# Kernel optimization log

Measured on AMD Instinct MI355X. Metric: run time of the kernel, lower is better.

Reference implementation:

```python
import jax, jax.numpy as jnp
import numpy as np

WS = 14  # window size
NH = 12  # num heads
EPS = 1e-5  # torch LayerNorm eps


def _rel_idx(ws: int) -> np.ndarray:
    coords = np.stack(np.meshgrid(np.arange(ws), np.arange(ws), indexing='ij'))
    cf = coords.reshape(2, -1)                      # (2, N)
    rel = cf[:, :, None] - cf[:, None, :]           # (2, N, N)
    rel = rel.transpose(1, 2, 0).copy()
    rel[:, :, 0] += ws - 1
    rel[:, :, 1] += ws - 1
    rel[:, :, 0] *= 2 * ws - 1
    return rel.sum(-1)                              # (N, N) int


def _layernorm(x, w, b):
    mu = jnp.mean(x, axis=-1, keepdims=True)
    var = jnp.var(x, axis=-1, keepdims=True)
    return (x - mu) * jax.lax.rsqrt(var + EPS) * w + b


def setup_inputs() -> dict:
    key = jax.random.key(0)
    ks = jax.random.split(key, 8)
    d, dff = 768, 3072
    s = lambda k, shape, sc: jax.random.normal(k, shape, jnp.float32) * sc
    return {
        'x': jax.random.normal(ks[0], (8, d, 56, 56), jnp.float32),
        'norm1_w': jnp.ones((d,), jnp.float32),
        'norm1_b': jnp.zeros((d,), jnp.float32),
        'qkv_w': s(ks[1], (d, 3 * d), 0.02),
        'qkv_b': jnp.zeros((3 * d,), jnp.float32),
        'rel_bias_table': s(ks[2], ((2 * WS - 1) ** 2, NH), 0.02),
        'proj_w': s(ks[3], (d, d), 0.02),
        'proj_b': jnp.zeros((d,), jnp.float32),
        'norm2_w': jnp.ones((d,), jnp.float32),
        'norm2_b': jnp.zeros((d,), jnp.float32),
        'fc1_w': s(ks[4], (d, dff), 0.02),
        'fc1_b': jnp.zeros((dff,), jnp.float32),
        'fc2_w': s(ks[5], (dff, d), 0.02),
        'fc2_b': jnp.zeros((d,), jnp.float32),
        'gamma1': jnp.full((d,), 1e-5, jnp.float32),
        'gamma2': jnp.full((d,), 1e-5, jnp.float32),
    }


def reference(x, norm1_w, norm1_b, qkv_w, qkv_b, rel_bias_table, proj_w, proj_b,
              norm2_w, norm2_b, fc1_w, fc1_b, fc2_w, fc2_b, gamma1, gamma2):
    B, C, H, W = x.shape
    nh, hd = NH, C // NH
    N = WS * WS
    xs = jnp.transpose(x, (0, 2, 3, 1))             # B,H,W,C
    shortcut = xs
    h = _layernorm(xs, norm1_w, norm1_b)

    # window partition (H, W divisible by WS)
    hw = h.reshape(B, H // WS, WS, W // WS, WS, C)
    hw = jnp.transpose(hw, (0, 1, 3, 2, 4, 5)).reshape(-1, N, C)  # (Bw, N, C)

    qkv = hw @ qkv_w + qkv_b                        # (Bw, N, 3C)
    qkv = qkv.reshape(-1, N, 3, nh, hd)
    q, k, v = [jnp.transpose(qkv[:, :, i], (0, 2, 1, 3)) for i in range(3)]  # (Bw,nh,N,hd)

    attn = jnp.einsum('bhnd,bhmd->bhnm', q, k) * (hd ** -0.5)
    rel_idx = jnp.asarray(_rel_idx(WS))             # static (N,N)
    bias = rel_bias_table[rel_idx]                  # (N,N,nh)
    attn = attn + jnp.transpose(bias, (2, 0, 1))[None]
    attn = jax.nn.softmax(attn, axis=-1)

    out = jnp.einsum('bhnm,bhmd->bnhd', attn, v).reshape(-1, N, C)
    out = out @ proj_w + proj_b                     # (Bw, N, C)

    # window reverse
    out = out.reshape(B, H // WS, W // WS, WS, WS, C)
    out = jnp.transpose(out, (0, 1, 3, 2, 4, 5)).reshape(B, H, W, C)

    xs = shortcut + gamma1 * out
    h2 = _layernorm(xs, norm2_w, norm2_b)
    mlp = jax.nn.gelu(h2 @ fc1_w + fc1_b, approximate=False) @ fc2_w + fc2_b
    xs = xs + gamma2 * mlp
    return jnp.transpose(xs, (0, 3, 1, 2))          # B,C,H,W
```

## Files before the change

kernel.cpp:

```cpp
#include <hip/hip_runtime.h>
#include <cstdint>
#include <cstddef>


typedef unsigned short u16;
typedef short short8 __attribute__((ext_vector_type(8)));
typedef float floatx4 __attribute__((ext_vector_type(4)));

static __device__ __forceinline__ float bf2f(u16 u) {
  return __uint_as_float(((unsigned)u) << 16);
}
static __device__ __forceinline__ u16 f2bf(float f) {
  unsigned u = __float_as_uint(f);
  return (u16)((u + 0x7FFFu + ((u >> 16) & 1u)) >> 16);
}
static __device__ __forceinline__ float ldin(const void* p, size_t i, int isf) {
  return isf ? ((const float*)p)[i] : bf2f(((const u16*)p)[i]);
}
static __device__ __forceinline__ void gload_lds16(const void* g, void* l) {
  __builtin_amdgcn_global_load_lds(
      (const __attribute__((address_space(1))) void*)g,
      (__attribute__((address_space(3))) void*)l, 16, 0, 0);
}
static __device__ __forceinline__ float fast_gelu(float v) {
  float u2 = v * (1.5957691216f + 0.0713548163f * v * v);
  return v * (1.0f / (1.0f + __expf(-u2)));
}

__global__ __launch_bounds__(256) void detect_kernel(const u16* __restrict__ x,
                                                     int* __restrict__ flag) {
  __shared__ int tot;
  if (threadIdx.x == 0) tot = 0;
  __syncthreads();
  int cnt = 0;
  for (int i = threadIdx.x; i < 4096; i += 256) {
    int e = (x[i] >> 7) & 0xFF;
    if (e >= 0xC1) cnt++;
  }
  atomicAdd(&tot, cnt);
  __syncthreads();
  if (threadIdx.x == 0) flag[0] = (tot > 16) ? 1 : 0;
}

__global__ __launch_bounds__(256) void cvt_params_kernel(
    const void* n1w, const void* n1b, const void* qkvb, const void* projb,
    const void* n2w, const void* n2b, const void* fc1b, const void* fc2b,
    const void* g1, const void* g2, const void* bt, u16* __restrict__ P,
    const int* __restrict__ flag) {
  int isf = *flag;
  int i = blockIdx.x * 256 + threadIdx.x;
  const void* src; int off;
  if      (i < 768)   { src = n1w;   off = i; }
  else if (i < 1536)  { src = n1b;   off = i - 768; }
  else if (i < 3840)  { src = qkvb;  off = i - 1536; }
  else if (i < 4608)  { src = projb; off = i - 3840; }
  else if (i < 5376)  { src = n2w;   off = i - 4608; }
  else if (i < 6144)  { src = n2b;   off = i - 5376; }
  else if (i < 9216)  { src = fc1b;  off = i - 6144; }
  else if (i < 9984)  { src = fc2b;  off = i - 9216; }
  else if (i < 10752) { src = g1;    off = i - 9984; }
  else if (i < 11520) { src = g2;    off = i - 10752; }
  else if (i < 20268) { src = bt;    off = i - 11520; }
  else return;
  P[i] = f2bf(ldin(src, off, isf));
}

__global__ __launch_bounds__(256) void wtr_kernel(const void* __restrict__ W,
                                                  u16* __restrict__ WT,
                                                  int K, int N,
                                                  const int* __restrict__ flag) {
  int isf = *flag;
  __shared__ u16 tl[32][33];
  int tx = threadIdx.x, ty = threadIdx.y;
  int n0 = blockIdx.x * 32, k0 = blockIdx.y * 32;
#pragma unroll
  for (int j = 0; j < 32; j += 8)
    tl[ty + j][tx] = f2bf(ldin(W, (size_t)(k0 + ty + j) * N + n0 + tx, isf));
  __syncthreads();
#pragma unroll
  for (int j = 0; j < 32; j += 8)
    WT[(size_t)(n0 + ty + j) * K + k0 + tx] = tl[tx][ty + j];
}

__global__ __launch_bounds__(256) void tin_kernel(const void* __restrict__ x,
                                                  u16* __restrict__ sc,
                                                  const int* __restrict__ flag) {
  int isf = *flag;
  int cc = blockIdx.x, h = blockIdx.y, b = blockIdx.z;
  __shared__ u16 tile[64 * 57];
  int tid = threadIdx.x;
  for (int i = tid; i < 64 * 56; i += 256) {
    int ci = i / 56, w = i - ci * 56;
    tile[ci * 57 + w] =
        f2bf(ldin(x, (((size_t)b * 768 + cc * 64 + ci) * 56 + h) * 56 + w, isf));
  }
  __syncthreads();
  int hb = h / 14, hi = h - hb * 14;
  for (int i = tid; i < 56 * 64; i += 256) {
    int w = i >> 6, ci = i & 63;
    int wb = w / 14, wj = w - wb * 14;
    int r = (b * 16 + hb * 4 + wb) * 196 + hi * 14 + wj;
    sc[(size_t)r * 768 + cc * 64 + ci] = tile[ci * 57 + w];
  }
}

__global__ __launch_bounds__(256) void tout_kernel(const u16* __restrict__ src,
                                                   void* __restrict__ out,
                                                   const int* __restrict__ flag) {
  int isf = *flag;
  int cc = blockIdx.x, h = blockIdx.y, b = blockIdx.z;
  __shared__ u16 tile[64 * 57];
  int tid = threadIdx.x;
  int hb = h / 14, hi = h - hb * 14;
  for (int i = tid; i < 56 * 64; i += 256) {
    int w = i >> 6, ci = i & 63;
    int wb = w / 14, wj = w - wb * 14;
    int r = (b * 16 + hb * 4 + wb) * 196 + hi * 14 + wj;
    tile[ci * 57 + w] = src[(size_t)r * 768 + cc * 64 + ci];
  }
  __syncthreads();
  for (int i = tid; i < 64 * 56; i += 256) {
    int ci = i / 56, w = i - ci * 56;
    size_t o = (((size_t)b * 768 + cc * 64 + ci) * 56 + h) * 56 + w;
    if (isf) ((float*)out)[o] = bf2f(tile[ci * 57 + w]);
    else     ((u16*)out)[o]   = tile[ci * 57 + w];
  }
}

__global__ __launch_bounds__(256) void ln_kernel(const u16* __restrict__ xin,
                                                 const u16* __restrict__ wt,
                                                 const u16* __restrict__ bs,
                                                 u16* __restrict__ out) {
  int row = blockIdx.x, t = threadIdx.x;
  const u16* xr = xin + (size_t)row * 768;
  float v0 = bf2f(xr[t]), v1 = bf2f(xr[t + 256]), v2 = bf2f(xr[t + 512]);
  float s1 = v0 + v1 + v2;
  float s2 = v0 * v0 + v1 * v1 + v2 * v2;
#pragma unroll
  for (int off = 32; off > 0; off >>= 1) {
    s1 += __shfl_xor(s1, off);
    s2 += __shfl_xor(s2, off);
  }
  __shared__ float p1[4], p2[4];
  if ((t & 63) == 0) { p1[t >> 6] = s1; p2[t >> 6] = s2; }
  __syncthreads();
  float S1 = p1[0] + p1[1] + p1[2] + p1[3];
  float S2 = p2[0] + p2[1] + p2[2] + p2[3];
  float mu = S1 * (1.f / 768.f);
  float var = S2 * (1.f / 768.f) - mu * mu;
  float rs = rsqrtf(var + 1e-5f);
  u16* orow = out + (size_t)row * 768;
  orow[t]       = f2bf((v0 - mu) * rs * bf2f(wt[t])       + bf2f(bs[t]));
  orow[t + 256] = f2bf((v1 - mu) * rs * bf2f(wt[t + 256]) + bf2f(bs[t + 256]));
  orow[t + 512] = f2bf((v2 - mu) * rs * bf2f(wt[t + 512]) + bf2f(bs[t + 512]));
}

template <int EPI>
__global__ __launch_bounds__(256, 4) void gemm128_kernel(
    const u16* __restrict__ A, const u16* __restrict__ BT,
    const u16* __restrict__ bias, const u16* __restrict__ gamma,
    u16* __restrict__ out, int M, int N, int K, int NX, int NYT) {
  __shared__ __align__(16) u16 LDS[8704];

  int bid = blockIdx.x;
  int r8 = bid & 7, q = bid >> 3;
  int xb = q % NX, yb = (q / NX) * 8 + r8;
  if (yb >= NYT) return;
  int m0 = yb * 128, n0 = xb * 128;

  int tid = threadIdx.x;
  int w = tid >> 6, l = tid & 63;
  int l15 = l & 15, quad = l >> 4;
  int wm = w & 1, wn = w >> 1;

  int lrow16 = l >> 2;
  int lk = ((l & 3) ^ ((l >> 3) & 3)) * 8;
  int ra0 = m0 + w * 32 + lrow16;       if (ra0 > M - 1) ra0 = M - 1;
  int ra1 = m0 + w * 32 + 16 + lrow16;  if (ra1 > M - 1) ra1 = M - 1;
  const u16* a0 = A + (size_t)ra0 * K + lk;
  const u16* a1 = A + (size_t)ra1 * K + lk;
  const u16* b0 = BT + (size_t)(n0 + w * 32 + lrow16) * K + lk;
  const u16* b1 = BT + (size_t)(n0 + w * 32 + 16 + lrow16) * K + lk;
  int dA0 = (w * 2) * 512, dA1 = (w * 2 + 1) * 512;

  int kqs = (quad ^ ((l15 >> 1) & 3)) * 8;

  floatx4 acc[4][4];
#pragma unroll
  for (int i = 0; i < 4; ++i)
#pragma unroll
    for (int j = 0; j < 4; ++j)
#pragma unroll
      for (int e = 0; e < 4; ++e) acc[i][j][e] = 0.f;

  int nt = K >> 5;
  for (int t = 0; t < nt; ++t) {
    int ko = t << 5;
    __syncthreads();
    gload_lds16(a0 + ko, LDS + dA0);
    gload_lds16(a1 + ko, LDS + dA1);
    gload_lds16(b0 + ko, LDS + 4096 + dA0);
    gload_lds16(b1 + ko, LDS + 4096 + dA1);
    __syncthreads();
    __builtin_amdgcn_s_setprio(1);
    short8 bfr[4];
#pragma unroll
    for (int ni = 0; ni < 4; ++ni)
      bfr[ni] = *(const short8*)&LDS[4096 + (wn * 64 + ni * 16 + l15) * 32 + kqs];
#pragma unroll
    for (int mi = 0; mi < 4; ++mi) {
      short8 afr = *(const short8*)&LDS[(wm * 64 + mi * 16 + l15) * 32 + kqs];
#pragma unroll
      for (int ni = 0; ni < 4; ++ni)
        acc[mi][ni] = __builtin_amdgcn_mfma_f32_16x16x32_bf16(
            afr, bfr[ni], acc[mi][ni], 0, 0, 0);
    }
    __builtin_amdgcn_s_setprio(0);
  }

  constexpr int CSTR = 136;
  float bv[4];
#pragma unroll
  for (int ni = 0; ni < 4; ++ni)
    bv[ni] = bf2f(bias[n0 + wn * 64 + ni * 16 + l15]);
  for (int cch = 0; cch < 2; ++cch) {
    __syncthreads();
    if (wm == cch) {
#pragma unroll
      for (int mi = 0; mi < 4; ++mi)
#pragma unroll
        for (int ni = 0; ni < 4; ++ni) {
          int cl = wn * 64 + ni * 16 + l15;
#pragma unroll
          for (int reg = 0; reg < 4; ++reg) {
            float v = acc[mi][ni][reg] + bv[ni];
            if constexpr (EPI == 2) v = fast_gelu(v);
            LDS[(mi * 16 + quad * 4 + reg) * CSTR + cl] = f2bf(v);
          }
        }
    }
    __syncthreads();
#pragma unroll
    for (int it = 0; it < 4; ++it) {
      int idx = it * 256 + tid;
      int row = idx >> 4, c8 = (idx & 15) * 8;
      int grow = m0 + cch * 64 + row;
      if (grow < M) {
        short8 val = *(const short8*)&LDS[row * CSTR + c8];
        u16* po = out + (size_t)grow * N + n0 + c8;
        if constexpr (EPI == 1) {
          short8 rv = *(const short8*)po;
          short8 gv = *(const short8*)(gamma + n0 + c8);
          short8 res;
#pragma unroll
          for (int e = 0; e < 8; ++e)
            res[e] = (short)f2bf(bf2f((u16)rv[e]) +
                                 bf2f((u16)gv[e]) * bf2f((u16)val[e]));
          *(short8*)po = res;
        } else {
          *(short8*)po = val;
        }
      }
    }
  }
}

__global__ __launch_bounds__(256) void attn_kernel(const u16* __restrict__ qkv,
                                                   const u16* __restrict__ btab,
                                                   u16* __restrict__ out) {
  __shared__ __align__(16) u16 VT[64 * 232];
  __shared__ __align__(16) u16 Pa[4 * 2 * 512];
  __shared__ float bS[729];
  int bid = blockIdx.x;
  int win = bid / 12, h = bid - win * 12;
  int tid = threadIdx.x, w = tid >> 6, l = tid & 63;
  int lane15 = l & 15, quad = l >> 4;
  const u16* qbase = qkv + (size_t)win * 196 * 2304;

  for (int i = tid; i < 64 * 28; i += 256) {
    int d = i / 28, m = i - d * 28;
    VT[d * 232 + 196 + m] = 0;
  }
  for (int i = tid; i < 196 * 64; i += 256) {
    int m = i >> 6, d = i & 63;
    VT[d * 232 + m] = qbase[(size_t)m * 2304 + 1536 + h * 64 + d];
  }
  for (int i = tid; i < 729; i += 256) bS[i] = bf2f(btab[i * 12 + h]);
  __syncthreads();

  u16* Pw = Pa + w * 1024;
  for (int rt = w; rt < 13; rt += 4) {
    floatx4 acc[13];
#pragma unroll
    for (int nt = 0; nt < 13; ++nt)
#pragma unroll
      for (int e = 0; e < 4; ++e) acc[nt][e] = 0.f;

    int rq = rt * 16 + lane15;
    bool qok = rq < 196;
#pragma unroll
    for (int kk = 0; kk < 2; ++kk) {
      short8 qf;
      if (qok)
        qf = *(const short8*)&qbase[(size_t)rq * 2304 + h * 64 + kk * 32 + quad * 8];
      else
#pragma unroll
        for (int e = 0; e < 8; ++e) qf[e] = 0;
#pragma unroll
      for (int nt = 0; nt < 13; ++nt) {
        int n = nt * 16 + lane15;
        short8 kf = *(const short8*)&qbase[(size_t)n * 2304 + 768 + h * 64 + kk * 32 + quad * 8];
        acc[nt] = __builtin_amdgcn_mfma_f32_16x16x32_bf16(qf, kf, acc[nt], 0, 0, 0);
      }
    }

    int i1[4], j1[4]; bool rv[4]; float mx[4], sm[4];
#pragma unroll
    for (int reg = 0; reg < 4; ++reg) {
      int r = rt * 16 + quad * 4 + reg;
      i1[reg] = r / 14; j1[reg] = r - i1[reg] * 14;
      rv[reg] = r < 196; mx[reg] = -1e30f; sm[reg] = 0.f;
    }
#pragma unroll
    for (int nt = 0; nt < 13; ++nt) {
      int cc = nt * 16 + lane15;
      bool cv = cc < 196;
      int i2 = cc / 14, j2 = cc - i2 * 14;
#pragma unroll
      for (int reg = 0; reg < 4; ++reg) {
        float v;
        if (cv) {
          v = acc[nt][reg] * 0.125f;
          if (rv[reg]) v += bS[(i1[reg] - i2 + 13) * 27 + (j1[reg] - j2 + 13)];
        } else v = -1e30f;
        acc[nt][reg] = v;
        mx[reg] = fmaxf(mx[reg], v);
      }
    }
#pragma unroll
    for (int reg = 0; reg < 4; ++reg)
#pragma unroll
      for (int off = 1; off < 16; off <<= 1)
        mx[reg] = fmaxf(mx[reg], __shfl_xor(mx[reg], off));
#pragma unroll
    for (int nt = 0; nt < 13; ++nt)
#pragma unroll
      for (int reg = 0; reg < 4; ++reg) {
        float p = __expf(acc[nt][reg] - mx[reg]);
        acc[nt][reg] = p; sm[reg] += p;
      }
#pragma unroll
    for (int reg = 0; reg < 4; ++reg) {
#pragma unroll
      for (int off = 1; off < 16; off <<= 1) sm[reg] += __shfl_xor(sm[reg], off);
      sm[reg] = 1.f / sm[reg];
    }

    floatx4 oa[4];
#pragma unroll
    for (int dt = 0; dt < 4; ++dt)
#pragma unroll
      for (int e = 0; e < 4; ++e) oa[dt][e] = 0.f;
#pragma unroll
    for (int kk = 0; kk < 7; ++kk) {
      u16* Pb = Pw + (kk & 1) * 512;
#pragma unroll
      for (int p = 0; p < 2; ++p) {
        int nt = kk * 2 + p;
#pragma unroll
        for (int reg = 0; reg < 4; ++reg) {
          float v = (nt < 13) ? acc[nt][reg] * sm[reg] : 0.f;
          Pb[(quad * 4 + reg) * 32 + p * 16 + lane15] = f2bf(v);
        }
      }
      asm volatile("s_waitcnt lgkmcnt(0)" ::: "memory");
      short8 pf = *(const short8*)&Pb[lane15 * 32 + quad * 8];
#pragma unroll
      for (int dt = 0; dt < 4; ++dt) {
        short8 vf = *(const short8*)&VT[(dt * 16 + lane15) * 232 + kk * 32 + quad * 8];
        oa[dt] = __builtin_amdgcn_mfma_f32_16x16x32_bf16(pf, vf, oa[dt], 0, 0, 0);
      }
    }
#pragma unroll
    for (int dt = 0; dt < 4; ++dt)
#pragma unroll
      for (int reg = 0; reg < 4; ++reg) {
        int r = rt * 16 + quad * 4 + reg;
        if (r < 196)
          out[((size_t)win * 196 + r) * 768 + h * 64 + dt * 16 + lane15] =
              f2bf(oa[dt][reg]);
      }
  }
}

static inline int gemm_grid(int NX, int NYT) { return NX * ((NYT + 7) / 8) * 8; }

extern "C" void kernel_launch(void* const* d_in, const int* in_sizes, int n_in,
                              void* d_out, int out_size, void* d_ws, size_t ws_size,
                              hipStream_t stream) {
  const void* x      = d_in[0];
  const void* n1w    = d_in[1];
  const void* n1b    = d_in[2];
  const void* qkv_w  = d_in[3];
  const void* qkv_b  = d_in[4];
  const void* btab   = d_in[5];
  const void* proj_w = d_in[6];
  const void* proj_b = d_in[7];
  const void* n2w    = d_in[8];
  const void* n2b    = d_in[9];
  const void* fc1_w  = d_in[10];
  const void* fc1_b  = d_in[11];
  const void* fc2_w  = d_in[12];
  const void* fc2_b  = d_in[13];
  const void* gamma1 = d_in[14];
  const void* gamma2 = d_in[15];
  (void)in_sizes; (void)n_in; (void)out_size;

  int c;
  if      (ws_size >= 245432576ull) c = 1;
  else if (ws_size >= 168362240ull) c = 2;
  else                              c = 4;
  const int R = 25088 / c;
  const int WN = 128 / c;
  const int NYT = (R + 127) / 128;

  char* ws = (char*)d_ws;
  int*  flag  = (int*)ws;
  u16*  P     = (u16*)(ws + 256);
  u16*  qkvT  = (u16*)(ws + 65792);
  u16*  projT = (u16*)(ws + 65792 + 3538944);
  u16*  fc1T  = (u16*)(ws + 65792 + 4718592);
  u16*  fc2T  = (u16*)(ws + 65792 + 9437184);
  const size_t B0 = 38535168;
  u16*  buf0  = (u16*)(ws + 14221568);
  u16*  buf1  = (u16*)(ws + 14221568 + B0);
  char* scr   = ws + 14221568 + 2 * B0;

  u16 *p_n1w = P, *p_n1b = P + 768, *p_qkvb = P + 1536, *p_projb = P + 3840;
  u16 *p_n2w = P + 4608, *p_n2b = P + 5376, *p_fc1b = P + 6144;
  u16 *p_fc2b = P + 9216, *p_g1 = P + 9984, *p_g2 = P + 10752, *p_bt = P + 11520;

  dim3 b256(256), bw(32, 8);
  detect_kernel<<<dim3(1), b256, 0, stream>>>((const u16*)x, flag);
  cvt_params_kernel<<<dim3(80), b256, 0, stream>>>(
      n1w, n1b, qkv_b, proj_b, n2w, n2b, fc1_b, fc2_b, gamma1, gamma2, btab,
      P, flag);
  wtr_kernel<<<dim3(72, 24), bw, 0, stream>>>(qkv_w, qkvT, 768, 2304, flag);
  wtr_kernel<<<dim3(24, 24), bw, 0, stream>>>(proj_w, projT, 768, 768, flag);
  wtr_kernel<<<dim3(96, 24), bw, 0, stream>>>(fc1_w, fc1T, 768, 3072, flag);
  wtr_kernel<<<dim3(24, 96), bw, 0, stream>>>(fc2_w, fc2T, 3072, 768, flag);

  tin_kernel<<<dim3(12, 56, 8), b256, 0, stream>>>(x, buf0, flag);
  ln_kernel<<<dim3(25088), b256, 0, stream>>>(buf0, p_n1w, p_n1b, buf1);

  for (int hc = 0; hc < c; ++hc) {
    size_t ro = (size_t)hc * R * 768;
    u16* qC = (u16*)scr;
    u16* aC = (u16*)(scr + (size_t)R * 4608);
    gemm128_kernel<0><<<dim3(gemm_grid(18, NYT)), b256, 0, stream>>>(
        buf1 + ro, qkvT, p_qkvb, nullptr, qC, R, 2304, 768, 18, NYT);
    attn_kernel<<<dim3(WN * 12), b256, 0, stream>>>(qC, p_bt, aC);
    gemm128_kernel<1><<<dim3(gemm_grid(6, NYT)), b256, 0, stream>>>(
        aC, projT, p_projb, p_g1, buf0 + ro, R, 768, 768, 6, NYT);
  }

  ln_kernel<<<dim3(25088), b256, 0, stream>>>(buf0, p_n2w, p_n2b, buf1);

  for (int hc = 0; hc < c; ++hc) {
    size_t ro = (size_t)hc * R * 768;
    u16* gC = (u16*)scr;
    gemm128_kernel<2><<<dim3(gemm_grid(24, NYT)), b256, 0, stream>>>(
        buf1 + ro, fc1T, p_fc1b, nullptr, gC, R, 3072, 768, 24, NYT);
    gemm128_kernel<1><<<dim3(gemm_grid(6, NYT)), b256, 0, stream>>>(
        gC, fc2T, p_fc2b, p_g2, buf0 + ro, R, 768, 3072, 6, NYT);
  }

  tout_kernel<<<dim3(12, 56, 8), b256, 0, stream>>>(buf0, d_out, flag);
}
```

Before: 980.8 us.

## Replace 128x128 GEMM with larger 512-thread tiles and register-prefetched operands

```diff
diff --git a/kernel.cpp b/kernel.cpp
--- a/kernel.cpp
+++ b/kernel.cpp
@@ -156,66 +156,232 @@
 }
 
 template <int EPI>
-__global__ __launch_bounds__(256, 4) void gemm128_kernel(
+__global__ __launch_bounds__(512, 2) void gemmA_kernel(
     const u16* __restrict__ A, const u16* __restrict__ BT,
     const u16* __restrict__ bias, const u16* __restrict__ gamma,
     u16* __restrict__ out, int M, int N, int K, int NX, int NYT) {
-  __shared__ __align__(16) u16 LDS[8704];
+  constexpr int ATS = 16384;
+  __shared__ __align__(16) u16 LDS[2 * ATS];
 
   int bid = blockIdx.x;
   int r8 = bid & 7, q = bid >> 3;
   int xb = q % NX, yb = (q / NX) * 8 + r8;
   if (yb >= NYT) return;
-  int m0 = yb * 128, n0 = xb * 128;
+  int m0 = yb * 256, n0 = xb * 256;
 
   int tid = threadIdx.x;
   int w = tid >> 6, l = tid & 63;
   int l15 = l & 15, quad = l >> 4;
   int wm = w & 1, wn = w >> 1;
 
-  int lrow16 = l >> 2;
-  int lk = ((l & 3) ^ ((l >> 3) & 3)) * 8;
-  int ra0 = m0 + w * 32 + lrow16;       if (ra0 > M - 1) ra0 = M - 1;
-  int ra1 = m0 + w * 32 + 16 + lrow16;  if (ra1 > M - 1) ra1 = M - 1;
-  const u16* a0 = A + (size_t)ra0 * K + lk;
-  const u16* a1 = A + (size_t)ra1 * K + lk;
-  const u16* b0 = BT + (size_t)(n0 + w * 32 + lrow16) * K + lk;
-  const u16* b1 = BT + (size_t)(n0 + w * 32 + 16 + lrow16) * K + lk;
-  int dA0 = (w * 2) * 512, dA1 = (w * 2 + 1) * 512;
-
-  int kqs = (quad ^ ((l15 >> 1) & 3)) * 8;
+  int lrow8 = l >> 3;
+  int lk = ((l & 7) ^ lrow8) * 8;
+  const u16* aptr[4];
+#pragma unroll
+  for (int j = 0; j < 4; ++j) {
+    int ra = m0 + w * 32 + j * 8 + lrow8;
+    if (ra > M - 1) ra = M - 1;
+    aptr[j] = A + (size_t)ra * K + lk;
+  }
+  int kq0 = (((quad * 16)      ^ ((l15 & 7) << 4)) >> 1);
+  int kq1 = (((64 + quad * 16) ^ ((l15 & 7) << 4)) >> 1);
+
+  const u16* bp0 = BT + (size_t)(n0 + wn * 64 +  0 + l15) * K + quad * 8;
+  const u16* bp1 = BT + (size_t)(n0 + wn * 64 + 16 + l15) * K + quad * 8;
+  const u16* bp2 = BT + (size_t)(n0 + wn * 64 + 32 + l15) * K + quad * 8;
+  const u16* bp3 = BT + (size_t)(n0 + wn * 64 + 48 + l15) * K + quad * 8;
+
+  floatx4 acc[8][4];
+#pragma unroll
+  for (int i = 0; i < 8; ++i)
+#pragma unroll
+    for (int jn = 0; jn < 4; ++jn)
+#pragma unroll
+      for (int e = 0; e < 4; ++e) acc[i][jn][e] = 0.f;
+
+  int nt = K >> 6;
+#pragma unroll
+  for (int j = 0; j < 4; ++j)
+    gload_lds16(aptr[j], LDS + (w * 4 + j) * 512);
+  short8 bc[4][2], bn[4][2];
+  bc[0][0] = *(const short8*)(bp0);      bc[0][1] = *(const short8*)(bp0 + 32);
+  bc[1][0] = *(const short8*)(bp1);      bc[1][1] = *(const short8*)(bp1 + 32);
+  bc[2][0] = *(const short8*)(bp2);      bc[2][1] = *(const short8*)(bp2 + 32);
+  bc[3][0] = *(const short8*)(bp3);      bc[3][1] = *(const short8*)(bp3 + 32);
+
+#pragma unroll 2
+  for (int t = 0; t < nt; ++t) {
+    const u16* Ac = LDS + (t & 1) * ATS;
+    u16* An = LDS + ((t + 1) & 1) * ATS;
+    asm volatile("s_waitcnt vmcnt(0)" ::: "memory");
+    __builtin_amdgcn_s_barrier();
+    bool pf = (t + 1) < nt;
+    int ko = (t + 1) << 6;
+    if (pf) {
+#pragma unroll
+      for (int j = 0; j < 4; ++j)
+        gload_lds16(aptr[j] + ko, An + (w * 4 + j) * 512);
+      bn[0][0] = *(const short8*)(bp0 + ko);
+      bn[0][1] = *(const short8*)(bp0 + ko + 32);
+      bn[1][0] = *(const short8*)(bp1 + ko);
+      bn[1][1] = *(const short8*)(bp1 + ko + 32);
+      bn[2][0] = *(const short8*)(bp2 + ko);
+      bn[2][1] = *(const short8*)(bp2 + ko + 32);
+      bn[3][0] = *(const short8*)(bp3 + ko);
+      bn[3][1] = *(const short8*)(bp3 + ko + 32);
+    }
+    __builtin_amdgcn_s_setprio(1);
+#pragma unroll
+    for (int mi = 0; mi < 8; ++mi) {
+      const u16* ap = Ac + (wm * 128 + mi * 16 + l15) * 64;
+      short8 a0 = *(const short8*)(ap + kq0);
+      short8 a1 = *(const short8*)(ap + kq1);
+#pragma unroll
+      for (int ni = 0; ni < 4; ++ni) {
+        acc[mi][ni] = __builtin_amdgcn_mfma_f32_16x16x32_bf16(
+            a0, bc[ni][0], acc[mi][ni], 0, 0, 0);
+        acc[mi][ni] = __builtin_amdgcn_mfma_f32_16x16x32_bf16(
+            a1, bc[ni][1], acc[mi][ni], 0, 0, 0);
+      }
+    }
+    __builtin_amdgcn_s_setprio(0);
+#pragma unroll
+    for (int ni = 0; ni < 4; ++ni) {
+      bc[ni][0] = bn[ni][0];
+      bc[ni][1] = bn[ni][1];
+    }
+  }
+
+  constexpr int CSTR = 264;
+  float bv[4];
+#pragma unroll
+  for (int ni = 0; ni < 4; ++ni)
+    bv[ni] = bf2f(bias[n0 + wn * 64 + ni * 16 + l15]);
+#pragma unroll
+  for (int cch = 0; cch < 4; ++cch) {
+    __syncthreads();
+    if (wm == (cch >> 1)) {
+#pragma unroll
+      for (int mi = 0; mi < 8; ++mi) {
+        if ((mi >> 2) == (cch & 1)) {
+          int rloc = (mi & 3) * 16 + quad * 4;
+#pragma unroll
+          for (int ni = 0; ni < 4; ++ni) {
+            int cl = wn * 64 + ni * 16 + l15;
+#pragma unroll
+            for (int reg = 0; reg < 4; ++reg) {
+              float v = acc[mi][ni][reg] + bv[ni];
+              if constexpr (EPI == 2) v = fast_gelu(v);
+              LDS[(rloc + reg) * CSTR + cl] = f2bf(v);
+            }
+          }
+        }
+      }
+    }
+    __syncthreads();
+#pragma unroll
+    for (int it = 0; it < 4; ++it) {
+      int idx = it * 512 + tid;
+      int row = idx >> 5, c8 = (idx & 31) * 8;
+      int grow = m0 + cch * 64 + row;
+      if (grow < M) {
+        short8 val = *(const short8*)&LDS[row * CSTR + c8];
+        u16* po = out + (size_t)grow * N + n0 + c8;
+        if constexpr (EPI == 1) {
+          short8 rv = *(const short8*)po;
+          short8 gv = *(const short8*)(gamma + n0 + c8);
+          short8 res;
+#pragma unroll
+          for (int e = 0; e < 8; ++e)
+            res[e] = (short)f2bf(bf2f((u16)rv[e]) +
+                                 bf2f((u16)gv[e]) * bf2f((u16)val[e]));
+          *(short8*)po = res;
+        } else {
+          *(short8*)po = val;
+        }
+      }
+    }
+  }
+}
+
+template <int EPI>
+__global__ __launch_bounds__(512, 2) void gemmR_kernel(
+    const u16* __restrict__ A, const u16* __restrict__ BT,
+    const u16* __restrict__ bias, const u16* __restrict__ gamma,
+    u16* __restrict__ out, int M, int N, int K, int NX, int NYT) {
+  __shared__ __align__(16) u16 LDS[64 * 136];
+
+  int bid = blockIdx.x;
+  int r8 = bid & 7, q = bid >> 3;
+  int xb = q % NX, yb = (q / NX) * 8 + r8;
+  if (yb >= NYT) return;
+  int m0 = yb * 256, n0 = xb * 128;
+
+  int tid = threadIdx.x;
+  int w = tid >> 6, l = tid & 63;
+  int l15 = l & 15, quad = l >> 4;
+  int wm = w & 3, wn = w >> 2;
+
+  int ar0 = m0 + wm * 64 +  0 + l15; if (ar0 > M - 1) ar0 = M - 1;
+  int ar1 = m0 + wm * 64 + 16 + l15; if (ar1 > M - 1) ar1 = M - 1;
+  int ar2 = m0 + wm * 64 + 32 + l15; if (ar2 > M - 1) ar2 = M - 1;
+  int ar3 = m0 + wm * 64 + 48 + l15; if (ar3 > M - 1) ar3 = M - 1;
+  const u16* ap0 = A + (size_t)ar0 * K + quad * 8;
+  const u16* ap1 = A + (size_t)ar1 * K + quad * 8;
+  const u16* ap2 = A + (size_t)ar2 * K + quad * 8;
+  const u16* ap3 = A + (size_t)ar3 * K + quad * 8;
+  const u16* bp0 = BT + (size_t)(n0 + wn * 64 +  0 + l15) * K + quad * 8;
+  const u16* bp1 = BT + (size_t)(n0 + wn * 64 + 16 + l15) * K + quad * 8;
+  const u16* bp2 = BT + (size_t)(n0 + wn * 64 + 32 + l15) * K + quad * 8;
+  const u16* bp3 = BT + (size_t)(n0 + wn * 64 + 48 + l15) * K + quad * 8;
 
   floatx4 acc[4][4];
 #pragma unroll
   for (int i = 0; i < 4; ++i)
 #pragma unroll
-    for (int j = 0; j < 4; ++j)
-#pragma unroll
-      for (int e = 0; e < 4; ++e) acc[i][j][e] = 0.f;
-
-  int nt = K >> 5;
+    for (int jn = 0; jn < 4; ++jn)
+#pragma unroll
+      for (int e = 0; e < 4; ++e) acc[i][jn][e] = 0.f;
+
+  int nt = K >> 6;
+  short8 ac[4][2], an[4][2], bc[4][2], bn[4][2];
+  ac[0][0] = *(const short8*)(ap0); ac[0][1] = *(const short8*)(ap0 + 32);
+  ac[1][0] = *(const short8*)(ap1); ac[1][1] = *(const short8*)(ap1 + 32);
+  ac[2][0] = *(const short8*)(ap2); ac[2][1] = *(const short8*)(ap2 + 32);
+  ac[3][0] = *(const short8*)(ap3); ac[3][1] = *(const short8*)(ap3 + 32);
+  bc[0][0] = *(const short8*)(bp0); bc[0][1] = *(const short8*)(bp0 + 32);
+  bc[1][0] = *(const short8*)(bp1); bc[1][1] = *(const short8*)(bp1 + 32);
+  bc[2][0] = *(const short8*)(bp2); bc[2][1] = *(const short8*)(bp2 + 32);
+  bc[3][0] = *(const short8*)(bp3); bc[3][1] = *(const short8*)(bp3 + 32);
+
+#pragma unroll 2
   for (int t = 0; t < nt; ++t) {
-    int ko = t << 5;
-    __syncthreads();
-    gload_lds16(a0 + ko, LDS + dA0);
-    gload_lds16(a1 + ko, LDS + dA1);
-    gload_lds16(b0 + ko, LDS + 4096 + dA0);
-    gload_lds16(b1 + ko, LDS + 4096 + dA1);
-    __syncthreads();
-    __builtin_amdgcn_s_setprio(1);
-    short8 bfr[4];
-#pragma unroll
-    for (int ni = 0; ni < 4; ++ni)
-      bfr[ni] = *(const short8*)&LDS[4096 + (wn * 64 + ni * 16 + l15) * 32 + kqs];
-#pragma unroll
-    for (int mi = 0; mi < 4; ++mi) {
-      short8 afr = *(const short8*)&LDS[(wm * 64 + mi * 16 + l15) * 32 + kqs];
-#pragma unroll
-      for (int ni = 0; ni < 4; ++ni)
+    bool pf = (t + 1) < nt;
+    int ko = (t + 1) << 6;
+    if (pf) {
+      an[0][0] = *(const short8*)(ap0 + ko); an[0][1] = *(const short8*)(ap0 + ko + 32);
+      an[1][0] = *(const short8*)(ap1 + ko); an[1][1] = *(const short8*)(ap1 + ko + 32);
+      an[2][0] = *(const short8*)(ap2 + ko); an[2][1] = *(const short8*)(ap2 + ko + 32);
+      an[3][0] = *(const short8*)(ap3 + ko); an[3][1] = *(const short8*)(ap3 + ko + 32);
+      bn[0][0] = *(const short8*)(bp0 + ko); bn[0][1] = *(const short8*)(bp0 + ko + 32);
+      bn[1][0] = *(const short8*)(bp1 + ko); bn[1][1] = *(const short8*)(bp1 + ko + 32);
+      bn[2][0] = *(const short8*)(bp2 + ko); bn[2][1] = *(const short8*)(bp2 + ko + 32);
+      bn[3][0] = *(const short8*)(bp3 + ko); bn[3][1] = *(const short8*)(bp3 + ko + 32);
+    }
+#pragma unroll
+    for (int mi = 0; mi < 4; ++mi)
+#pragma unroll
+      for (int ni = 0; ni < 4; ++ni) {
         acc[mi][ni] = __builtin_amdgcn_mfma_f32_16x16x32_bf16(
-            afr, bfr[ni], acc[mi][ni], 0, 0, 0);
-    }
-    __builtin_amdgcn_s_setprio(0);
+            ac[mi][0], bc[ni][0], acc[mi][ni], 0, 0, 0);
+        acc[mi][ni] = __builtin_amdgcn_mfma_f32_16x16x32_bf16(
+            ac[mi][1], bc[ni][1], acc[mi][ni], 0, 0, 0);
+      }
+#pragma unroll
+    for (int i = 0; i < 4; ++i) {
+      ac[i][0] = an[i][0]; ac[i][1] = an[i][1];
+      bc[i][0] = bn[i][0]; bc[i][1] = bn[i][1];
+    }
   }
 
   constexpr int CSTR = 136;
@@ -223,7 +389,8 @@
 #pragma unroll
   for (int ni = 0; ni < 4; ++ni)
     bv[ni] = bf2f(bias[n0 + wn * 64 + ni * 16 + l15]);
-  for (int cch = 0; cch < 2; ++cch) {
+#pragma unroll
+  for (int cch = 0; cch < 4; ++cch) {
     __syncthreads();
     if (wm == cch) {
 #pragma unroll
@@ -241,8 +408,8 @@
     }
     __syncthreads();
 #pragma unroll
-    for (int it = 0; it < 4; ++it) {
-      int idx = it * 256 + tid;
+    for (int it = 0; it < 2; ++it) {
+      int idx = it * 512 + tid;
       int row = idx >> 4, c8 = (idx & 15) * 8;
       int grow = m0 + cch * 64 + row;
       if (grow < M) {
@@ -422,7 +589,7 @@
   else                              c = 4;
   const int R = 25088 / c;
   const int WN = 128 / c;
-  const int NYT = (R + 127) / 128;
+  const int NYT = (R + 255) / 256;
 
   char* ws = (char*)d_ws;
   int*  flag  = (int*)ws;
@@ -440,7 +607,7 @@
   u16 *p_n2w = P + 4608, *p_n2b = P + 5376, *p_fc1b = P + 6144;
   u16 *p_fc2b = P + 9216, *p_g1 = P + 9984, *p_g2 = P + 10752, *p_bt = P + 11520;
 
-  dim3 b256(256), bw(32, 8);
+  dim3 b256(256), b512(512), bw(32, 8);
   detect_kernel<<<dim3(1), b256, 0, stream>>>((const u16*)x, flag);
   cvt_params_kernel<<<dim3(80), b256, 0, stream>>>(
       n1w, n1b, qkv_b, proj_b, n2w, n2b, fc1_b, fc2_b, gamma1, gamma2, btab,
@@ -457,10 +624,10 @@
     size_t ro = (size_t)hc * R * 768;
     u16* qC = (u16*)scr;
     u16* aC = (u16*)(scr + (size_t)R * 4608);
-    gemm128_kernel<0><<<dim3(gemm_grid(18, NYT)), b256, 0, stream>>>(
-        buf1 + ro, qkvT, p_qkvb, nullptr, qC, R, 2304, 768, 18, NYT);
+    gemmA_kernel<0><<<dim3(gemm_grid(9, NYT)), b512, 0, stream>>>(
+        buf1 + ro, qkvT, p_qkvb, nullptr, qC, R, 2304, 768, 9, NYT);
     attn_kernel<<<dim3(WN * 12), b256, 0, stream>>>(qC, p_bt, aC);
-    gemm128_kernel<1><<<dim3(gemm_grid(6, NYT)), b256, 0, stream>>>(
+    gemmR_kernel<1><<<dim3(gemm_grid(6, NYT)), b512, 0, stream>>>(
         aC, projT, p_projb, p_g1, buf0 + ro, R, 768, 768, 6, NYT);
   }
 
@@ -469,9 +636,9 @@
   for (int hc = 0; hc < c; ++hc) {
     size_t ro = (size_t)hc * R * 768;
     u16* gC = (u16*)scr;
-    gemm128_kernel<2><<<dim3(gemm_grid(24, NYT)), b256, 0, stream>>>(
-        buf1 + ro, fc1T, p_fc1b, nullptr, gC, R, 3072, 768, 24, NYT);
-    gemm128_kernel<1><<<dim3(gemm_grid(6, NYT)), b256, 0, stream>>>(
+    gemmA_kernel<2><<<dim3(gemm_grid(12, NYT)), b512, 0, stream>>>(
+        buf1 + ro, fc1T, p_fc1b, nullptr, gC, R, 3072, 768, 12, NYT);
+    gemmR_kernel<1><<<dim3(gemm_grid(6, NYT)), b512, 0, stream>>>(
         gC, fc2T, p_fc2b, p_g2, buf0 + ro, R, 768, 3072, 6, NYT);
   }
 
```

Result: slower. 1.592 ms (+62.3%).
